# Kernel optimization log

Hardware: AMD Instinct MI355X
Metric: run time of the kernel (lower is better)

## Reference

```python
import jax, jax.numpy as jnp
import numpy as np

H, W, D_F, N, BINS = 64, 64, 768, 16, 16
SPAN = 1.0
CLIP = 3.0


def _make_bin_idx(h, w, bins):
    # torch _fftfreq_1d == np.fft.fftfreq (k/n with negative wrap)
    fx = np.fft.fftfreq(h).astype(np.float32)
    fy = np.fft.fftfreq(w).astype(np.float32)
    r = np.sqrt(fx[:, None] ** 2 + fy[None, :] ** 2)  # (h, w)
    edges = np.linspace(r.min(), r.max() + 1e-12, bins + 1, dtype=np.float32)
    # torch.bucketize(r, edges[1:-1], right=False) == searchsorted side='left'
    idx = np.searchsorted(edges[1:-1], r, side='left')
    return np.clip(idx, 0, bins - 1).astype(np.int32)


def setup_inputs() -> dict:
    key = jax.random.key(0)
    x = jax.random.normal(key, (N, D_F, H, W), dtype=jnp.float32)
    # parameter init exactly as torch __init__ (bins>1, span>0 branch)
    g_init = np.linspace(-SPAN, SPAN, BINS, dtype=np.float32)
    deltas = np.clip(g_init[1:] - g_init[:-1], 1e-6, None)
    raw_deltas = np.log(np.expm1(deltas)).astype(np.float32)  # inverse softplus
    g1 = np.float32(g_init[0])
    bin_idx_2d = _make_bin_idx(H, W, BINS)
    return {
        "x": x,
        "g1": jnp.asarray(g1),
        "raw_deltas": jnp.asarray(raw_deltas),
        "bin_idx_2d": jnp.asarray(bin_idx_2d),
    }


def _sqrt_lambda(g1, raw_deltas, bin_idx_2d):
    # monotone bin values g_b = g1 + cumsum(softplus(raw_deltas))
    deltas = jax.nn.softplus(raw_deltas)
    g = jnp.concatenate([g1[None], g1[None] + jnp.cumsum(deltas)], axis=0)  # (bins,)
    ell = g[bin_idx_2d]                      # (h, w) log-lambda per frequency
    ell = ell - ell.mean()                   # logdet gauge centering
    ell = jnp.clip(ell, -CLIP, CLIP)
    lam = jnp.exp(ell)
    # logdet gauge: normalize geometric mean to 1 (clip may break centering)
    lam = lam / jnp.maximum(jnp.exp(jnp.log(lam).mean()), 1e-12)
    return jnp.sqrt(lam)


def reference(x, g1, raw_deltas, bin_idx_2d):
    sqrt_lam = _sqrt_lambda(g1, raw_deltas, bin_idx_2d).astype(x.dtype)
    X = jnp.fft.fft2(x, norm="ortho")                    # (n, d_f, h, w) complex
    y = jnp.fft.ifft2(X * sqrt_lam[None, None, :, :], norm="ortho").real
    return y.astype(x.dtype)
```

## Files before the change

kernel.cpp:

```cpp
#include <hip/hip_runtime.h>
#include <math.h>


__device__ __forceinline__ float2 cadd(float2 a, float2 b){ return make_float2(a.x+b.x, a.y+b.y); }
__device__ __forceinline__ float2 csub(float2 a, float2 b){ return make_float2(a.x-b.x, a.y-b.y); }
__device__ __forceinline__ float2 cmul(float2 a, float2 b){ return make_float2(a.x*b.x - a.y*b.y, a.x*b.y + a.y*b.x); }
__device__ __forceinline__ float2 cmulc(float2 a, float2 b){
  return make_float2(a.x*b.x + a.y*b.y, a.y*b.x - a.x*b.y);
}

template<int SGN>
__device__ __forceinline__ float2 crot(float2 a){
  return (SGN < 0) ? make_float2(a.y, -a.x) : make_float2(-a.y, a.x);
}

template<int SGN>
__device__ __forceinline__ void fft8(float2 a[8]){
  const float s = 0.70710678118654752440f;
  float2 e0=a[0], e1=a[2], e2=a[4], e3=a[6];
  float2 o0=a[1], o1=a[3], o2=a[5], o3=a[7];
  float2 t0=cadd(e0,e2), t1=csub(e0,e2), t2=cadd(e1,e3), t3=crot<SGN>(csub(e1,e3));
  float2 E0=cadd(t0,t2), E2=csub(t0,t2), E1=cadd(t1,t3), E3=csub(t1,t3);
  float2 u0=cadd(o0,o2), u1=csub(o0,o2), u2=cadd(o1,o3), u3=crot<SGN>(csub(o1,o3));
  float2 O0=cadd(u0,u2), O2=csub(u0,u2), O1=cadd(u1,u3), O3=csub(u1,u3);
  const float2 w1 = make_float2( s, (SGN < 0) ? -s : s);
  const float2 w3 = make_float2(-s, (SGN < 0) ? -s : s);
  O1 = cmul(O1, w1);
  O2 = crot<SGN>(O2);
  O3 = cmul(O3, w3);
  a[0]=cadd(E0,O0); a[4]=csub(E0,O0);
  a[1]=cadd(E1,O1); a[5]=csub(E1,O1);
  a[2]=cadd(E2,O2); a[6]=csub(E2,O2);
  a[3]=cadd(E3,O3); a[7]=csub(E3,O3);
}

__device__ __forceinline__ void lds_sync(){
  __builtin_amdgcn_fence(__ATOMIC_ACQ_REL, "wavefront");
  __builtin_amdgcn_wave_barrier();
  __builtin_amdgcn_fence(__ATOMIC_ACQ_REL, "wavefront");
}

__device__ __forceinline__ void build_tw(int t, float2 tw[8]){
  float sv, cv;
  __sincosf(-(float)M_PI * (float)t / 32.0f, &sv, &cv);
  const float2 wstep = make_float2(cv, sv);
  tw[0] = make_float2(1.f, 0.f);
  #pragma unroll
  for (int j = 1; j < 8; ++j) tw[j] = cmul(tw[j-1], wstep);
}

__global__ void filter_kernel(const float* __restrict__ g1p,
                              const float* __restrict__ rawd,
                              const int*   __restrict__ bidx,
                              float*       __restrict__ Sperm){
  __shared__ float gsh[16];
  __shared__ float red[256];
  const int tid = threadIdx.x;
  if (tid == 0){
    float g = g1p[0];
    gsh[0] = g;
    for (int b = 0; b < 15; ++b){
      float d = rawd[b];
      float sp = (d > 20.f) ? d : log1pf(expf(d));
      g += sp;
      gsh[b+1] = g;
    }
  }
  __syncthreads();
  float ell[16];
  float sacc = 0.f;
  #pragma unroll
  for (int i = 0; i < 16; ++i){
    int p = tid + 256*i;
    ell[i] = gsh[bidx[p]];
    sacc += ell[i];
  }
  red[tid] = sacc; __syncthreads();
  for (int off = 128; off > 0; off >>= 1){
    if (tid < off) red[tid] += red[tid + off];
    __syncthreads();
  }
  float mean1 = red[0] * (1.f/4096.f);
  __syncthreads();
  sacc = 0.f;
  #pragma unroll
  for (int i = 0; i < 16; ++i){
    float e = ell[i] - mean1;
    e = fminf(fmaxf(e, -3.f), 3.f);
    ell[i] = e;
    sacc += e;
  }
  red[tid] = sacc; __syncthreads();
  for (int off = 128; off > 0; off >>= 1){
    if (tid < off) red[tid] += red[tid + off];
    __syncthreads();
  }
  float mean2 = red[0] * (1.f/4096.f);
  #pragma unroll
  for (int i = 0; i < 16; ++i){
    int p = tid + 256*i;
    int h = p >> 6, w = p & 63;
    float val = expf(0.5f * (ell[i] - mean2)) * (1.0f/4096.0f);
    int pw = ((w & 7) << 3) | (w >> 3);
    Sperm[h*64 + pw] = val;
  }
}

__global__ __launch_bounds__(512, 4) void spectral_kernel(
    const float* __restrict__ x, const float* __restrict__ Sp, float* __restrict__ y)
{
  __shared__ float2 tile[64*66];
  float4* tile4 = reinterpret_cast<float4*>(tile);
  const int tid = threadIdx.x;
  const int wv = tid >> 6;
  const int l  = tid & 63;
  const int o  = l & 7;
  const int u  = l >> 3;
  const int g  = (wv << 3) + o;
  const int tA = u;
  const int c  = (wv << 3) + o;
  const int tB = ((u & 1) << 2) | (u & 2) | (u >> 2);
  const int mB = (tB < 4) ? tB : (tB ^ 1);

  const long long baseA = (long long)blockIdx.x * 8192;
  const float* xA = x + baseA;
  const float* xB = xA + 4096;
  float* yA = y + baseA;
  float* yB = yA + 4096;

  float2 tw[8];

  build_tw(tA, tw);
  {
    const float* rA = xA + (g << 6);
    const float* rB = xB + (g << 6);
    float2 a[8];
    #pragma unroll
    for (int j = 0; j < 8; ++j) a[j] = make_float2(rA[tA + 8*j], rB[tA + 8*j]);
    fft8<-1>(a);
    #pragma unroll
    for (int j = 1; j < 8; ++j) a[j] = cmul(a[j], tw[j]);
    #pragma unroll
    for (int q = 0; q < 4; ++q)
      tile4[33*g + 4*tA + q] = make_float4(a[2*q].x, a[2*q].y, a[2*q+1].x, a[2*q+1].y);
    lds_sync();
    #pragma unroll
    for (int j = 0; j < 8; ++j) a[j] = tile[66*g + 8*j + tA];
    fft8<-1>(a);
    lds_sync();
    #pragma unroll
    for (int q = 0; q < 4; ++q)
      tile4[33*g + 4*tA + q] = make_float4(a[2*q].x, a[2*q].y, a[2*q+1].x, a[2*q+1].y);
  }
  __syncthreads();

  build_tw(tB, tw);
  {
    float2 a[8];
    #pragma unroll
    for (int j = 0; j < 8; ++j) a[j] = tile[66*(tB + 8*j) + c];
    fft8<-1>(a);
    #pragma unroll
    for (int j = 1; j < 8; ++j) a[j] = cmul(a[j], tw[j]);
    lds_sync();
    #pragma unroll
    for (int q = 0; q < 4; ++q){
      float2 lo = a[2*q], hi = a[2*q+1];
      if (q >= 2){ float2 t2 = lo; lo = hi; hi = t2; }
      tile4[33*(8*tB + o) + 4*wv + q] = make_float4(lo.x, lo.y, hi.x, hi.y);
    }
    lds_sync();
    #pragma unroll
    for (int j = 0; j < 8; ++j) a[j] = tile[66*(8*j + o) + 8*wv + mB];
    fft8<-1>(a);
    #pragma unroll
    for (int j = 0; j < 8; ++j){
      float f = Sp[((tB + 8*j) << 6) + c];
      a[j].x *= f; a[j].y *= f;
    }
    fft8<+1>(a);
    #pragma unroll
    for (int j = 1; j < 8; ++j) a[j] = cmulc(a[j], tw[j]);
    lds_sync();
    #pragma unroll
    for (int q = 0; q < 4; ++q){
      float2 lo = a[2*q], hi = a[2*q+1];
      if (q >= 2){ float2 t2 = lo; lo = hi; hi = t2; }
      tile4[33*(8*tB + o) + 4*wv + q] = make_float4(lo.x, lo.y, hi.x, hi.y);
    }
    lds_sync();
    #pragma unroll
    for (int j = 0; j < 8; ++j) a[j] = tile[66*(8*j + o) + 8*wv + mB];
    fft8<+1>(a);
    lds_sync();
    #pragma unroll
    for (int j = 0; j < 8; ++j) tile[66*(tB + 8*j) + c] = a[j];
  }
  __syncthreads();

  build_tw(tA, tw);
  {
    float2 a[8];
    #pragma unroll
    for (int q = 0; q < 4; ++q){
      float4 v = tile4[33*g + 4*tA + q];
      a[2*q]   = make_float2(v.x, v.y);
      a[2*q+1] = make_float2(v.z, v.w);
    }
    fft8<+1>(a);
    #pragma unroll
    for (int j = 1; j < 8; ++j) a[j] = cmulc(a[j], tw[j]);
    lds_sync();
    #pragma unroll
    for (int q = 0; q < 4; ++q)
      tile4[33*g + 4*tA + q] = make_float4(a[2*q].x, a[2*q].y, a[2*q+1].x, a[2*q+1].y);
    lds_sync();
    #pragma unroll
    for (int j = 0; j < 8; ++j) a[j] = tile[66*g + 8*j + tA];
    fft8<+1>(a);
    float* pA = yA + (g << 6) + tA;
    float* pB = yB + (g << 6) + tA;
    #pragma unroll
    for (int j = 0; j < 8; ++j){ pA[8*j] = a[j].x; pB[8*j] = a[j].y; }
  }
}

extern "C" void kernel_launch(void* const* d_in, const int* in_sizes, int n_in,
                              void* d_out, int out_size, void* d_ws, size_t ws_size,
                              hipStream_t stream){
  (void)in_sizes; (void)n_in; (void)out_size; (void)ws_size;
  const float* x    = (const float*)d_in[0];
  const float* g1   = (const float*)d_in[1];
  const float* rawd = (const float*)d_in[2];
  const int*   bidx = (const int*)d_in[3];
  float* y     = (float*)d_out;
  float* Sperm = (float*)d_ws;

  filter_kernel<<<dim3(1), dim3(256), 0, stream>>>(g1, rawd, bidx, Sperm);
  spectral_kernel<<<dim3(6144), dim3(512), 0, stream>>>(x, Sperm, y);
}
```

Baseline: 375.3 us.

## Make spectral kernel persistent over six image pairs with register prefetch

The grid shrinks from 6144 to 1024 blocks, and each block loops over six image pairs. The global loads for the next pair are issued into registers before the current pair's FFT work, so memory latency overlaps with compute. The aim is to hide load latency and cut block launch overhead. In exchange it adds 16 live registers per thread under the 512x4 launch bound, which risks spills or lower occupancy. It also leaves only 1024 blocks, which may underfill the GPU's CUs.

```diff
diff --git a/kernel.cpp b/kernel.cpp
--- a/kernel.cpp
+++ b/kernel.cpp
@@ -121,22 +121,30 @@
   const int c  = (wv << 3) + o;
   const int tB = ((u & 1) << 2) | (u & 2) | (u >> 2);
   const int mB = (tB < 4) ? tB : (tB ^ 1);
-
-  const long long baseA = (long long)blockIdx.x * 8192;
-  const float* xA = x + baseA;
-  const float* xB = xA + 4096;
-  float* yA = y + baseA;
-  float* yB = yA + 4096;
+  const int off = (g << 6) + tA;
 
   float2 tw[8];
-
-  build_tw(tA, tw);
+  float ldA[8], ldB[8];
+
   {
-    const float* rA = xA + (g << 6);
-    const float* rB = xB + (g << 6);
+    const float* p0 = x + ((long long)blockIdx.x << 13);
+    #pragma unroll
+    for (int j = 0; j < 8; ++j){ ldA[j] = p0[off + 8*j]; ldB[j] = p0[off + 4096 + 8*j]; }
+  }
+
+  #pragma unroll 1
+  for (int p = 0; p < 6; ++p){
     float2 a[8];
     #pragma unroll
-    for (int j = 0; j < 8; ++j) a[j] = make_float2(rA[tA + 8*j], rB[tA + 8*j]);
+    for (int j = 0; j < 8; ++j) a[j] = make_float2(ldA[j], ldB[j]);
+
+    if (p < 5){
+      const float* pn = x + ((long long)((p+1)*1024 + blockIdx.x) << 13);
+      #pragma unroll
+      for (int j = 0; j < 8; ++j){ ldA[j] = pn[off + 8*j]; ldB[j] = pn[off + 4096 + 8*j]; }
+    }
+
+    build_tw(tA, tw);
     fft8<-1>(a);
     #pragma unroll
     for (int j = 1; j < 8; ++j) a[j] = cmul(a[j], tw[j]);
@@ -151,12 +159,9 @@
     #pragma unroll
     for (int q = 0; q < 4; ++q)
       tile4[33*g + 4*tA + q] = make_float4(a[2*q].x, a[2*q].y, a[2*q+1].x, a[2*q+1].y);
-  }
-  __syncthreads();
-
-  build_tw(tB, tw);
-  {
-    float2 a[8];
+    __syncthreads();
+
+    build_tw(tB, tw);
     #pragma unroll
     for (int j = 0; j < 8; ++j) a[j] = tile[66*(tB + 8*j) + c];
     fft8<-1>(a);
@@ -195,12 +200,9 @@
     lds_sync();
     #pragma unroll
     for (int j = 0; j < 8; ++j) tile[66*(tB + 8*j) + c] = a[j];
-  }
-  __syncthreads();
-
-  build_tw(tA, tw);
-  {
-    float2 a[8];
+    __syncthreads();
+
+    build_tw(tA, tw);
     #pragma unroll
     for (int q = 0; q < 4; ++q){
       float4 v = tile4[33*g + 4*tA + q];
@@ -218,10 +220,15 @@
     #pragma unroll
     for (int j = 0; j < 8; ++j) a[j] = tile[66*g + 8*j + tA];
     fft8<+1>(a);
-    float* pA = yA + (g << 6) + tA;
-    float* pB = yB + (g << 6) + tA;
-    #pragma unroll
-    for (int j = 0; j < 8; ++j){ pA[8*j] = a[j].x; pB[8*j] = a[j].y; }
+    {
+      float* py = y + ((long long)(p*1024 + blockIdx.x) << 13);
+      #pragma unroll
+      for (int j = 0; j < 8; ++j){
+        py[off + 8*j]        = a[j].x;
+        py[off + 4096 + 8*j] = a[j].y;
+      }
+    }
+    lds_sync();
   }
 }
 
@@ -237,5 +244,5 @@
   float* Sperm = (float*)d_ws;
 
   filter_kernel<<<dim3(1), dim3(256), 0, stream>>>(g1, rawd, bidx, Sperm);
-  spectral_kernel<<<dim3(6144), dim3(512), 0, stream>>>(x, Sperm, y);
-}
+  spectral_kernel<<<dim3(1024), dim3(512), 0, stream>>>(x, Sperm, y);
+}
```

Result: no change. 376.2 us (+0.2%).
